# Optimization experiments

Hardware: AMD Instinct MI355X
Metric: run time of the kernel (lower is better)

Reference implementation:

```python
import jax, jax.numpy as jnp
import numpy as np

K = 3   # spatial_kernel_size
M = 5   # memory_size


def setup_inputs() -> dict:
    key = jax.random.key(0)
    ks = jax.random.split(key, 16)
    C = 64
    B, H, D, W = 2, 24, 24, 24
    s = 0.05
    n = jax.random.normal
    return {
        "x": n(ks[0], (B, C, H, D, W), jnp.float32),
        "prev_memory": jnp.zeros((B, C), jnp.float32),
        "Wq": n(ks[1], (C, C), jnp.float32) * s,
        "bq": n(ks[2], (C,), jnp.float32) * s,
        "Wk": n(ks[3], (C, C), jnp.float32) * s,
        "bk": n(ks[4], (C,), jnp.float32) * s,
        "Wv": n(ks[5], (C, C), jnp.float32) * s,
        "bv": n(ks[6], (C,), jnp.float32) * s,
        "mem_key": n(ks[7], (C, M), jnp.float32),
        "mem_value": n(ks[8], (C, M), jnp.float32),
        "Wg": n(ks[9], (C, 2 * C), jnp.float32) * s,
        "bg": n(ks[10], (C,), jnp.float32) * s,
        "W_ih": n(ks[11], (3 * C, C), jnp.float32) * s,
        "W_hh": n(ks[12], (3 * C, C), jnp.float32) * s,
        "b_ih": n(ks[13], (3 * C,), jnp.float32) * s,
        "b_hh": n(ks[14], (3 * C,), jnp.float32) * s,
    }


def _patches(x, k):
    # x: (B,C,H,D,W) -> (B,C,k^3,H,D,W) local neighborhoods (zero-padded)
    B, C, H, D, W = x.shape
    p = k // 2
    xp = jnp.pad(x, ((0, 0), (0, 0), (p, p), (p, p), (p, p)))
    sl = [xp[:, :, i:i + H, j:j + D, l:l + W]
          for i in range(k) for j in range(k) for l in range(k)]
    return jnp.stack(sl, axis=2)


def reference(x, prev_memory, Wq, bq, Wk, bk, Wv, bv, mem_key, mem_value,
              Wg, bg, W_ih, W_hh, b_ih, b_hh):
    B, C, H, D, W = x.shape
    N = H * D * W
    xf = x.reshape(B, C, N)
    pf = _patches(x, K).reshape(B, C, K ** 3, N)

    # 1x1x1 conv projections (pure channel mixes)
    q = jnp.einsum('oc,bcn->bon', Wq, xf) + bq[None, :, None]            # (B,C,N)
    k_sp = jnp.einsum('oc,bcmn->bomn', Wk, pf) + bk[None, :, None, None]  # (B,C,27,N)
    v_sp = jnp.einsum('oc,bcmn->bomn', Wv, pf) + bv[None, :, None, None]

    # memory tokens broadcast over all spatial locations
    k_mem = jnp.broadcast_to(mem_key[None, :, :, None], (B, C, M, N))
    v_mem = jnp.broadcast_to(mem_value[None, :, :, None], (B, C, M, N))
    kk = jnp.concatenate([k_mem, k_sp], axis=2)   # (B,C,M+27,N)
    vv = jnp.concatenate([v_mem, v_sp], axis=2)

    # per-channel scalar attention over memory+neighborhood axis
    attn = jax.nn.softmax(q[:, :, None, :] * kk / jnp.sqrt(jnp.float32(C)), axis=2)
    out = jnp.sum(attn * vv, axis=2).reshape(B, C, H, D, W)

    # sigmoid gate over concat([x, out])
    gin = jnp.concatenate([xf, out.reshape(B, C, N)], axis=1)  # (B,2C,N)
    gate = jax.nn.sigmoid(jnp.einsum('oc,bcn->bon', Wg, gin)
                          + bg[None, :, None]).reshape(B, C, H, D, W)
    out = gate * out + (1.0 - gate) * x

    # GRU memory update on spatially pooled features (torch GRUCell math)
    mu = out.mean(axis=(2, 3, 4))                 # (B,C)
    gi = mu @ W_ih.T + b_ih
    gh = prev_memory @ W_hh.T + b_hh
    ir, iz, ii = jnp.split(gi, 3, axis=1)
    hr, hz, hn = jnp.split(gh, 3, axis=1)
    r = jax.nn.sigmoid(ir + hr)
    z = jax.nn.sigmoid(iz + hz)
    ng = jnp.tanh(ii + r * hn)
    new_memory = (1.0 - z) * ng + z * prev_memory
    return out, new_memory
```

## Files before the change

### kernel.cpp

```cpp
#include <hip/hip_runtime.h>
#include <math.h>

#define NPOS 13824
#define CDIM 64
#define BTCH 2
#define LOG2E 1.4426950408889634f
#define QSCALE (0.125f * LOG2E)

__device__ __forceinline__ unsigned int f2bf1(float f) {
  unsigned int u = __float_as_uint(f);
  return (u + 0x7FFFu + ((u >> 16) & 1u)) >> 16;
}

__global__ __launch_bounds__(256) void qkvg_kernel(
    const float* __restrict__ x,
    const float* __restrict__ Wq, const float* __restrict__ bq,
    const float* __restrict__ Wk, const float* __restrict__ bk,
    const float* __restrict__ Wv, const float* __restrict__ bv,
    const float* __restrict__ Wg,
    unsigned int* __restrict__ KVp, float* __restrict__ QGX,
    float* __restrict__ pool)
{
  __shared__ __align__(16) float wqt[64*68];
  __shared__ __align__(16) float wkt[64*68];
  __shared__ __align__(16) float wvt[64*68];
  __shared__ __align__(16) float wgt[64*68];
  const int t  = threadIdx.x;
  const int bi = blockIdx.x;
  const int b  = bi / 216;
  const int n0 = (bi - b*216) * 64;
  if (bi == 0 && t < 128) pool[t] = 0.0f;

  #pragma unroll
  for (int k = 0; k < 16; ++k) {
    int idx = t + k*256;
    int lo = idx & 63, hi = idx >> 6;
    wqt[lo*68 + hi] = Wq[idx] * QSCALE;
    wkt[lo*68 + hi] = Wk[idx];
    wvt[lo*68 + hi] = Wv[idx];
    wgt[lo*68 + hi] = Wg[hi*128 + lo];
  }
  __syncthreads();

  const int c0  = (t & 15) * 4;
  const int nn0 = (t >> 4) * 4;
  const float* xbase = x + (size_t)(b*64)*NPOS + n0 + nn0;
  float aq[4][4] = {}; float ak[4][4] = {}; float av[4][4] = {}; float ag[4][4] = {};
  #pragma unroll 4
  for (int cp = 0; cp < 64; ++cp) {
    const float4 xv4 = *(const float4*)(xbase + (size_t)cp*NPOS);
    const float4 q4  = *(const float4*)&wqt[cp*68 + c0];
    const float4 k4  = *(const float4*)&wkt[cp*68 + c0];
    const float4 v4  = *(const float4*)&wvt[cp*68 + c0];
    const float4 g4  = *(const float4*)&wgt[cp*68 + c0];
    const float xa[4] = {xv4.x, xv4.y, xv4.z, xv4.w};
    const float qa[4] = {q4.x, q4.y, q4.z, q4.w};
    const float ka[4] = {k4.x, k4.y, k4.z, k4.w};
    const float va[4] = {v4.x, v4.y, v4.z, v4.w};
    const float ga[4] = {g4.x, g4.y, g4.z, g4.w};
    #pragma unroll
    for (int ci = 0; ci < 4; ++ci)
      #pragma unroll
      for (int ni = 0; ni < 4; ++ni) {
        aq[ci][ni] = fmaf(qa[ci], xa[ni], aq[ci][ni]);
        ak[ci][ni] = fmaf(ka[ci], xa[ni], ak[ci][ni]);
        av[ci][ni] = fmaf(va[ci], xa[ni], av[ci][ni]);
        ag[ci][ni] = fmaf(ga[ci], xa[ni], ag[ci][ni]);
      }
  }
  float4 xr[4];
  #pragma unroll
  for (int e = 0; e < 4; ++e)
    xr[e] = *(const float4*)(x + (size_t)(b*64 + c0 + e)*NPOS + n0 + nn0);
  const float xre[4][4] = {{xr[0].x,xr[0].y,xr[0].z,xr[0].w},
                           {xr[1].x,xr[1].y,xr[1].z,xr[1].w},
                           {xr[2].x,xr[2].y,xr[2].z,xr[2].w},
                           {xr[3].x,xr[3].y,xr[3].z,xr[3].w}};
  const float4 bq4 = *(const float4*)&bq[c0];
  const float4 bk4 = *(const float4*)&bk[c0];
  const float4 bv4 = *(const float4*)&bv[c0];
  const float bqa[4] = {bq4.x, bq4.y, bq4.z, bq4.w};
  const float bka[4] = {bk4.x, bk4.y, bk4.z, bk4.w};
  const float bva[4] = {bv4.x, bv4.y, bv4.z, bv4.w};
  #pragma unroll
  for (int ni = 0; ni < 4; ++ni) {
    const int p = b*NPOS + n0 + nn0 + ni;
    uint4 kv;
    kv.x = (f2bf1(ak[0][ni]+bka[0]) << 16) | f2bf1(av[0][ni]+bva[0]);
    kv.y = (f2bf1(ak[1][ni]+bka[1]) << 16) | f2bf1(av[1][ni]+bva[1]);
    kv.z = (f2bf1(ak[2][ni]+bka[2]) << 16) | f2bf1(av[2][ni]+bva[2]);
    kv.w = (f2bf1(ak[3][ni]+bka[3]) << 16) | f2bf1(av[3][ni]+bva[3]);
    *(uint4*)&KVp[p*64 + c0] = kv;
    unsigned pk0 = (f2bf1(fmaf(bqa[0], QSCALE, aq[0][ni])) << 16) | f2bf1(ag[0][ni]);
    unsigned pk1 = (f2bf1(fmaf(bqa[1], QSCALE, aq[1][ni])) << 16) | f2bf1(ag[1][ni]);
    unsigned pk2 = (f2bf1(fmaf(bqa[2], QSCALE, aq[2][ni])) << 16) | f2bf1(ag[2][ni]);
    unsigned pk3 = (f2bf1(fmaf(bqa[3], QSCALE, aq[3][ni])) << 16) | f2bf1(ag[3][ni]);
    float4 o;
    o = make_float4(__uint_as_float(pk0), xre[0][ni], __uint_as_float(pk1), xre[1][ni]);
    *(float4*)&QGX[(size_t)(p*64 + c0)*2]     = o;
    o = make_float4(__uint_as_float(pk2), xre[2][ni], __uint_as_float(pk3), xre[3][ni]);
    *(float4*)&QGX[(size_t)(p*64 + c0)*2 + 4] = o;
  }
}

__global__ __launch_bounds__(256) void attn_kernel(
    float* __restrict__ OT,
    const unsigned int* __restrict__ KVp,
    const float* __restrict__ QGX,
    const float* __restrict__ bk, const float* __restrict__ bv,
    const float* __restrict__ memk, const float* __restrict__ memv,
    const float* __restrict__ Wg, const float* __restrict__ bg,
    float* __restrict__ pool)
{
  __shared__ __align__(16) unsigned int kvbuf[64*129];
  __shared__ __align__(16) float alsA[256];
  __shared__ __align__(16) float alsB[256];
  const int t = threadIdx.x;
  const int c = t & 63;
  const int w = t >> 6;

  {
    float* wgt2 = (float*)kvbuf;
    #pragma unroll
    for (int k = 0; k < 16; ++k) {
      int u = t + k*256;
      int cp = u >> 6, j = u & 63;
      wgt2[j*65 + cp] = Wg[cp*128 + 64 + j];
    }
  }
  __syncthreads();
  unsigned int wg2p[32];
  {
    const float* wgt2 = (const float*)kvbuf;
    #pragma unroll
    for (int j2 = 0; j2 < 32; ++j2) {
      unsigned lo = f2bf1(wgt2[(2*j2)*65 + c]);
      unsigned hi = f2bf1(wgt2[(2*j2+1)*65 + c]);
      wg2p[j2] = lo | (hi << 16);
    }
  }
  float mk[5], mv[5];
  #pragma unroll
  for (int m = 0; m < 5; ++m) { mk[m] = memk[c*5 + m]; mv[m] = memv[c*5 + m]; }
  const float bg_c = bg[c];
  const unsigned bias_kv = (f2bf1(bk[c]) << 16) | f2bf1(bv[c]);
  __syncthreads();

  const int bi = (int)(blockIdx.x & 7) * 128 + (int)(blockIdx.x >> 3);
  const int b  = bi >> 9;
  const int tb = bi & 511;
  const int h0 = (tb >> 6) * 3;
  const int d0 = ((tb >> 3) & 7) * 3;
  const int w0 = (tb & 7) * 3;
  const int bN = b * NPOS;

  for (int u = t; u < 8000; u += 256) {
    const int pos = u >> 6;
    const int ph = pos / 25, pr = pos - ph*25;
    const int pd = pr / 5,  pw = pr - pd*5;
    const int hh = h0 - 1 + ph, dd = d0 - 1 + pd, ww = w0 - 1 + pw;
    const bool inb = ((unsigned)hh < 24u) && ((unsigned)dd < 24u) && ((unsigned)ww < 24u);
    unsigned kv = bias_kv;
    if (inb) kv = KVp[(size_t)(bN + hh*576 + dd*24 + ww)*64 + c];
    kvbuf[c*129 + pos] = kv;
  }
  __syncthreads();

  float pacc = 0.0f;
  for (int li = w; li < 27; li += 8) {
    const int liB0 = li + 4;
    const bool hasB = liB0 < 27;
    const int liB = hasB ? liB0 : li;

    const int lhA = li / 9,  lrA = li - lhA*9;
    const int ldA = lrA / 3, lwA = lrA - ldA*3;
    const int pA  = bN + (h0+lhA)*576 + (d0+ldA)*24 + (w0+lwA);
    const unsigned int* kvA = &kvbuf[c*129 + lhA*25 + ldA*5 + lwA];
    const int lhB = liB / 9,  lrB = liB - lhB*9;
    const int ldB = lrB / 3,  lwB = lrB - ldB*3;
    const int pB  = bN + (h0+lhB)*576 + (d0+ldB)*24 + (w0+lwB);
    const unsigned int* kvB = &kvbuf[c*129 + lhB*25 + ldB*5 + lwB];

    const float2 gqA = *(const float2*)&QGX[(size_t)(pA*64 + c)*2];
    const float2 gqB = *(const float2*)&QGX[(size_t)(pB*64 + c)*2];
    const unsigned uqA = __float_as_uint(gqA.x);
    const unsigned uqB = __float_as_uint(gqB.x);
    const float qA  = __uint_as_float(uqA & 0xFFFF0000u);
    const float gxA = __uint_as_float(uqA << 16);
    const float xvA = gqA.y;
    const float qB  = __uint_as_float(uqB & 0xFFFF0000u);
    const float gxB = __uint_as_float(uqB << 16);
    const float xvB = gqB.y;

    float sA0 = 0.f, sA1 = 0.f, oA0 = 0.f, oA1 = 0.f;
    float sB0 = 0.f, sB1 = 0.f, oB0 = 0.f, oB1 = 0.f;
    #pragma unroll
    for (int m = 0; m < 5; ++m) {
      const float pfA = __builtin_amdgcn_exp2f(qA * mk[m]);
      const float pfB = __builtin_amdgcn_exp2f(qB * mk[m]);
      if (m & 1) { sA1 += pfA; oA1 = fmaf(pfA, mv[m], oA1);
                   sB1 += pfB; oB1 = fmaf(pfB, mv[m], oB1); }
      else       { sA0 += pfA; oA0 = fmaf(pfA, mv[m], oA0);
                   sB0 += pfB; oB0 = fmaf(pfB, mv[m], oB0); }
    }
    #pragma unroll
    for (int i = 0; i < 3; ++i)
      #pragma unroll
      for (int j = 0; j < 3; ++j)
        #pragma unroll
        for (int l = 0; l < 3; ++l) {
          const int s4  = i*9 + j*3 + l;
          const int off = i*25 + j*5 + l;
          const unsigned a = kvA[off], bb2 = kvB[off];
          const float kA = __uint_as_float(a & 0xFFFF0000u);
          const float vA = __uint_as_float(a << 16);
          const float kB = __uint_as_float(bb2 & 0xFFFF0000u);
          const float vB = __uint_as_float(bb2 << 16);
          const float pfA = __builtin_amdgcn_exp2f(qA * kA);
          const float pfB = __builtin_amdgcn_exp2f(qB * kB);
          if (s4 & 1) { sA1 += pfA; oA1 = fmaf(pfA, vA, oA1);
                        sB1 += pfB; oB1 = fmaf(pfB, vB, oB1); }
          else        { sA0 += pfA; oA0 = fmaf(pfA, vA, oA0);
                        sB0 += pfB; oB0 = fmaf(pfB, vB, oB0); }
        }
    const float attA = (oA0 + oA1) * __builtin_amdgcn_rcpf(sA0 + sA1);
    const float attB = (oB0 + oB1) * __builtin_amdgcn_rcpf(sB0 + sB1);

    alsA[w*64 + c] = attA;
    alsB[w*64 + c] = attB;
    float gA0 = gxA + bg_c, gA1 = 0.f, gA2 = 0.f, gA3 = 0.f;
    float gB0 = gxB + bg_c, gB1 = 0.f, gB2 = 0.f, gB3 = 0.f;
    #pragma unroll
    for (int j4 = 0; j4 < 16; ++j4) {
      const float4 a4 = *(const float4*)&alsA[w*64 + j4*4];
      const float4 b4 = *(const float4*)&alsB[w*64 + j4*4];
      const unsigned pk0 = wg2p[2*j4], pk1 = wg2p[2*j4+1];
      const float w0f = __uint_as_float(pk0 << 16);
      const float w1f = __uint_as_float(pk0 & 0xFFFF0000u);
      const float w2f = __uint_as_float(pk1 << 16);
      const float w3f = __uint_as_float(pk1 & 0xFFFF0000u);
      gA0 = fmaf(w0f, a4.x, gA0); gB0 = fmaf(w0f, b4.x, gB0);
      gA1 = fmaf(w1f, a4.y, gA1); gB1 = fmaf(w1f, b4.y, gB1);
      gA2 = fmaf(w2f, a4.z, gA2); gB2 = fmaf(w2f, b4.z, gB2);
      gA3 = fmaf(w3f, a4.w, gA3); gB3 = fmaf(w3f, b4.w, gB3);
    }
    const float glA   = (gA0 + gA1) + (gA2 + gA3);
    const float glB   = (gB0 + gB1) + (gB2 + gB3);
    const float gateA = __builtin_amdgcn_rcpf(1.0f + __builtin_amdgcn_exp2f(-LOG2E * glA));
    const float gateB = __builtin_amdgcn_rcpf(1.0f + __builtin_amdgcn_exp2f(-LOG2E * glB));
    const float finA  = fmaf(gateA, attA - xvA, xvA);
    const float finB  = fmaf(gateB, attB - xvB, xvB);
    OT[pA*64 + c] = finA;
    pacc += finA;
    if (hasB) { OT[pB*64 + c] = finB; pacc += finB; }
  }

  alsA[t] = pacc;
  __syncthreads();
  if (t < 64) {
    float s = alsA[t] + alsA[64 + t] + alsA[128 + t] + alsA[192 + t];
    atomicAdd(&pool[b*64 + t], s);
  }
}

__global__ __launch_bounds__(256) void outpool_kernel(
    const float* __restrict__ OT, float* __restrict__ out,
    const float* __restrict__ pool, const float* __restrict__ prev,
    const float* __restrict__ W_ih, const float* __restrict__ W_hh,
    const float* __restrict__ b_ih, const float* __restrict__ b_hh,
    float* __restrict__ outmem)
{
  __shared__ __align__(16) float ls[64*65];
  __shared__ __align__(16) float mu[128];
  __shared__ float gi[384];
  __shared__ float gh[384];
  const int t  = threadIdx.x;
  const int bi = blockIdx.x;
  const int b  = bi / 216;
  const int n0 = (bi - b*216) * 64;
  #pragma unroll
  for (int i = 0; i < 16; ++i) {
    int u = i*256 + t;
    int pos = u >> 6, cc = u & 63;
    ls[cc*65 + pos] = OT[(size_t)(b*NPOS + n0 + pos)*64 + cc];
  }
  if (bi == 0 && t < 128) mu[t] = pool[t] * (1.0f / (float)NPOS);
  __syncthreads();
  #pragma unroll
  for (int i = 0; i < 16; ++i) {
    int u = i*256 + t;
    int cc = u >> 6, j = u & 63;
    out[(size_t)(b*64 + cc)*NPOS + n0 + j] = ls[cc*65 + j];
  }
  if (bi != 0) return;

  for (int r = t; r < 384; r += 256) {
    const int b2 = r / 192, j = r - b2*192;
    const float4* wi4 = (const float4*)(W_ih + (size_t)j*64);
    const float4* wh4 = (const float4*)(W_hh + (size_t)j*64);
    const float4* mu4 = (const float4*)(mu + b2*64);
    const float4* pv4 = (const float4*)(prev + b2*64);
    float sgi = b_ih[j], sgh = b_hh[j];
    #pragma unroll
    for (int k = 0; k < 16; ++k) {
      float4 wv = wi4[k], m4 = mu4[k];
      sgi = fmaf(wv.x, m4.x, sgi); sgi = fmaf(wv.y, m4.y, sgi);
      sgi = fmaf(wv.z, m4.z, sgi); sgi = fmaf(wv.w, m4.w, sgi);
      float4 hv = wh4[k], p4 = pv4[k];
      sgh = fmaf(hv.x, p4.x, sgh); sgh = fmaf(hv.y, p4.y, sgh);
      sgh = fmaf(hv.z, p4.z, sgh); sgh = fmaf(hv.w, p4.w, sgh);
    }
    gi[r] = sgi; gh[r] = sgh;
  }
  __syncthreads();
  if (t < 128) {
    const int b2 = t >> 6, cc = t & 63;
    float ir = gi[b2*192 + cc],       hr = gh[b2*192 + cc];
    float iz = gi[b2*192 + 64 + cc],  hz = gh[b2*192 + 64 + cc];
    float ii = gi[b2*192 + 128 + cc], hn = gh[b2*192 + 128 + cc];
    float rr = 1.0f / (1.0f + __builtin_amdgcn_exp2f(-LOG2E * (ir + hr)));
    float zz = 1.0f / (1.0f + __builtin_amdgcn_exp2f(-LOG2E * (iz + hz)));
    float ng = tanhf(ii + rr * hn);
    outmem[t] = (1.0f - zz) * ng + zz * prev[t];
  }
}

extern "C" void kernel_launch(void* const* d_in, const int* in_sizes, int n_in,
                              void* d_out, int out_size, void* d_ws, size_t ws_size,
                              hipStream_t stream) {
  const float* x    = (const float*)d_in[0];
  const float* prev = (const float*)d_in[1];
  const float* Wq   = (const float*)d_in[2];
  const float* bq   = (const float*)d_in[3];
  const float* Wk   = (const float*)d_in[4];
  const float* bk   = (const float*)d_in[5];
  const float* Wv   = (const float*)d_in[6];
  const float* bv   = (const float*)d_in[7];
  const float* memk = (const float*)d_in[8];
  const float* memv = (const float*)d_in[9];
  const float* Wg   = (const float*)d_in[10];
  const float* bg   = (const float*)d_in[11];
  const float* W_ih = (const float*)d_in[12];
  const float* W_hh = (const float*)d_in[13];
  const float* b_ih = (const float*)d_in[14];
  const float* b_hh = (const float*)d_in[15];

  float* out    = (float*)d_out;
  float* outmem = out + (size_t)BTCH*CDIM*NPOS;

  const size_t SZ = (size_t)BTCH*NPOS*CDIM;
  float* wsf        = (float*)d_ws;
  float* OT         = wsf;
  unsigned int* KVp = (unsigned int*)(wsf + SZ);
  float* QGX        = wsf + 2*SZ;
  float* pool       = wsf + 4*SZ;

  qkvg_kernel<<<BTCH*216, 256, 0, stream>>>(x, Wq, bq, Wk, bk, Wv, bv, Wg,
                                            KVp, QGX, pool);
  attn_kernel<<<BTCH*512, 256, 0, stream>>>(OT, KVp, QGX,
                                            bk, bv, memk, memv, Wg, bg, pool);
  outpool_kernel<<<BTCH*216, 256, 0, stream>>>(OT, out, pool, prev,
                                               W_ih, W_hh, b_ih, b_hh, outmem);
}
```

Measured before the change: 165.7 us.

## Move gate matmul from attention kernel into tiled output kernel with last-block GRU

Removes the per-position gate GEMV, weight packing and pooling from the attention kernel, which now only writes raw attention outputs. A new output kernel does the gate projection as a register-tiled 64x64 matmul from shared memory, applies the gated blend against x, writes the output in channel-major order and accumulates the pool sum. The GRU update runs in the last block to finish, detected with an atomic counter, replacing the separate block-0 path. The query and x-gate are now stored as fp32 in separate buffers instead of packed bf16, which adds memory traffic but raises precision and takes the gate work off the attention kernel.

```diff
diff --git a/kernel.cpp b/kernel.cpp
--- a/kernel.cpp
+++ b/kernel.cpp
@@ -18,8 +18,8 @@
     const float* __restrict__ Wk, const float* __restrict__ bk,
     const float* __restrict__ Wv, const float* __restrict__ bv,
     const float* __restrict__ Wg,
-    unsigned int* __restrict__ KVp, float* __restrict__ QGX,
-    float* __restrict__ pool)
+    unsigned int* __restrict__ KVp, float* __restrict__ Qs,
+    float* __restrict__ GXCN, float* __restrict__ pool)
 {
   __shared__ __align__(16) float wqt[64*68];
   __shared__ __align__(16) float wkt[64*68];
@@ -29,7 +29,7 @@
   const int bi = blockIdx.x;
   const int b  = bi / 216;
   const int n0 = (bi - b*216) * 64;
-  if (bi == 0 && t < 128) pool[t] = 0.0f;
+  if (bi == 0 && t < 132) pool[t] = 0.0f;
 
   #pragma unroll
   for (int k = 0; k < 16; ++k) {
@@ -68,14 +68,6 @@
         ag[ci][ni] = fmaf(ga[ci], xa[ni], ag[ci][ni]);
       }
   }
-  float4 xr[4];
-  #pragma unroll
-  for (int e = 0; e < 4; ++e)
-    xr[e] = *(const float4*)(x + (size_t)(b*64 + c0 + e)*NPOS + n0 + nn0);
-  const float xre[4][4] = {{xr[0].x,xr[0].y,xr[0].z,xr[0].w},
-                           {xr[1].x,xr[1].y,xr[1].z,xr[1].w},
-                           {xr[2].x,xr[2].y,xr[2].z,xr[2].w},
-                           {xr[3].x,xr[3].y,xr[3].z,xr[3].w}};
   const float4 bq4 = *(const float4*)&bq[c0];
   const float4 bk4 = *(const float4*)&bk[c0];
   const float4 bv4 = *(const float4*)&bv[c0];
@@ -85,66 +77,39 @@
   #pragma unroll
   for (int ni = 0; ni < 4; ++ni) {
     const int p = b*NPOS + n0 + nn0 + ni;
+    float4 o;
+    o = make_float4(fmaf(bqa[0],QSCALE,aq[0][ni]), fmaf(bqa[1],QSCALE,aq[1][ni]),
+                    fmaf(bqa[2],QSCALE,aq[2][ni]), fmaf(bqa[3],QSCALE,aq[3][ni]));
+    *(float4*)&Qs[p*64 + c0] = o;
     uint4 kv;
     kv.x = (f2bf1(ak[0][ni]+bka[0]) << 16) | f2bf1(av[0][ni]+bva[0]);
     kv.y = (f2bf1(ak[1][ni]+bka[1]) << 16) | f2bf1(av[1][ni]+bva[1]);
     kv.z = (f2bf1(ak[2][ni]+bka[2]) << 16) | f2bf1(av[2][ni]+bva[2]);
     kv.w = (f2bf1(ak[3][ni]+bka[3]) << 16) | f2bf1(av[3][ni]+bva[3]);
     *(uint4*)&KVp[p*64 + c0] = kv;
-    unsigned pk0 = (f2bf1(fmaf(bqa[0], QSCALE, aq[0][ni])) << 16) | f2bf1(ag[0][ni]);
-    unsigned pk1 = (f2bf1(fmaf(bqa[1], QSCALE, aq[1][ni])) << 16) | f2bf1(ag[1][ni]);
-    unsigned pk2 = (f2bf1(fmaf(bqa[2], QSCALE, aq[2][ni])) << 16) | f2bf1(ag[2][ni]);
-    unsigned pk3 = (f2bf1(fmaf(bqa[3], QSCALE, aq[3][ni])) << 16) | f2bf1(ag[3][ni]);
-    float4 o;
-    o = make_float4(__uint_as_float(pk0), xre[0][ni], __uint_as_float(pk1), xre[1][ni]);
-    *(float4*)&QGX[(size_t)(p*64 + c0)*2]     = o;
-    o = make_float4(__uint_as_float(pk2), xre[2][ni], __uint_as_float(pk3), xre[3][ni]);
-    *(float4*)&QGX[(size_t)(p*64 + c0)*2 + 4] = o;
-  }
+  }
+  #pragma unroll
+  for (int ci = 0; ci < 4; ++ci)
+    *(float4*)&GXCN[(size_t)(b*64 + c0 + ci)*NPOS + n0 + nn0] =
+        make_float4(ag[ci][0], ag[ci][1], ag[ci][2], ag[ci][3]);
 }
 
 __global__ __launch_bounds__(256) void attn_kernel(
-    float* __restrict__ OT,
+    float* __restrict__ ATT,
+    const float* __restrict__ Qs,
     const unsigned int* __restrict__ KVp,
-    const float* __restrict__ QGX,
     const float* __restrict__ bk, const float* __restrict__ bv,
-    const float* __restrict__ memk, const float* __restrict__ memv,
-    const float* __restrict__ Wg, const float* __restrict__ bg,
-    float* __restrict__ pool)
+    const float* __restrict__ memk, const float* __restrict__ memv)
 {
   __shared__ __align__(16) unsigned int kvbuf[64*129];
-  __shared__ __align__(16) float alsA[256];
-  __shared__ __align__(16) float alsB[256];
   const int t = threadIdx.x;
   const int c = t & 63;
   const int w = t >> 6;
 
-  {
-    float* wgt2 = (float*)kvbuf;
-    #pragma unroll
-    for (int k = 0; k < 16; ++k) {
-      int u = t + k*256;
-      int cp = u >> 6, j = u & 63;
-      wgt2[j*65 + cp] = Wg[cp*128 + 64 + j];
-    }
-  }
-  __syncthreads();
-  unsigned int wg2p[32];
-  {
-    const float* wgt2 = (const float*)kvbuf;
-    #pragma unroll
-    for (int j2 = 0; j2 < 32; ++j2) {
-      unsigned lo = f2bf1(wgt2[(2*j2)*65 + c]);
-      unsigned hi = f2bf1(wgt2[(2*j2+1)*65 + c]);
-      wg2p[j2] = lo | (hi << 16);
-    }
-  }
   float mk[5], mv[5];
   #pragma unroll
   for (int m = 0; m < 5; ++m) { mk[m] = memk[c*5 + m]; mv[m] = memv[c*5 + m]; }
-  const float bg_c = bg[c];
   const unsigned bias_kv = (f2bf1(bk[c]) << 16) | f2bf1(bv[c]);
-  __syncthreads();
 
   const int bi = (int)(blockIdx.x & 7) * 128 + (int)(blockIdx.x >> 3);
   const int b  = bi >> 9;
@@ -166,7 +131,6 @@
   }
   __syncthreads();
 
-  float pacc = 0.0f;
   for (int li = w; li < 27; li += 8) {
     const int liB0 = li + 4;
     const bool hasB = liB0 < 27;
@@ -181,16 +145,8 @@
     const int pB  = bN + (h0+lhB)*576 + (d0+ldB)*24 + (w0+lwB);
     const unsigned int* kvB = &kvbuf[c*129 + lhB*25 + ldB*5 + lwB];
 
-    const float2 gqA = *(const float2*)&QGX[(size_t)(pA*64 + c)*2];
-    const float2 gqB = *(const float2*)&QGX[(size_t)(pB*64 + c)*2];
-    const unsigned uqA = __float_as_uint(gqA.x);
-    const unsigned uqB = __float_as_uint(gqB.x);
-    const float qA  = __uint_as_float(uqA & 0xFFFF0000u);
-    const float gxA = __uint_as_float(uqA << 16);
-    const float xvA = gqA.y;
-    const float qB  = __uint_as_float(uqB & 0xFFFF0000u);
-    const float gxB = __uint_as_float(uqB << 16);
-    const float xvB = gqB.y;
+    const float qA = Qs[pA*64 + c];
+    const float qB = Qs[pB*64 + c];
 
     float sA0 = 0.f, sA1 = 0.f, oA0 = 0.f, oA1 = 0.f;
     float sB0 = 0.f, sB1 = 0.f, oB0 = 0.f, oB1 = 0.f;
@@ -225,103 +181,133 @@
         }
     const float attA = (oA0 + oA1) * __builtin_amdgcn_rcpf(sA0 + sA1);
     const float attB = (oB0 + oB1) * __builtin_amdgcn_rcpf(sB0 + sB1);
-
-    alsA[w*64 + c] = attA;
-    alsB[w*64 + c] = attB;
-    float gA0 = gxA + bg_c, gA1 = 0.f, gA2 = 0.f, gA3 = 0.f;
-    float gB0 = gxB + bg_c, gB1 = 0.f, gB2 = 0.f, gB3 = 0.f;
-    #pragma unroll
-    for (int j4 = 0; j4 < 16; ++j4) {
-      const float4 a4 = *(const float4*)&alsA[w*64 + j4*4];
-      const float4 b4 = *(const float4*)&alsB[w*64 + j4*4];
-      const unsigned pk0 = wg2p[2*j4], pk1 = wg2p[2*j4+1];
-      const float w0f = __uint_as_float(pk0 << 16);
-      const float w1f = __uint_as_float(pk0 & 0xFFFF0000u);
-      const float w2f = __uint_as_float(pk1 << 16);
-      const float w3f = __uint_as_float(pk1 & 0xFFFF0000u);
-      gA0 = fmaf(w0f, a4.x, gA0); gB0 = fmaf(w0f, b4.x, gB0);
-      gA1 = fmaf(w1f, a4.y, gA1); gB1 = fmaf(w1f, b4.y, gB1);
-      gA2 = fmaf(w2f, a4.z, gA2); gB2 = fmaf(w2f, b4.z, gB2);
-      gA3 = fmaf(w3f, a4.w, gA3); gB3 = fmaf(w3f, b4.w, gB3);
-    }
-    const float glA   = (gA0 + gA1) + (gA2 + gA3);
-    const float glB   = (gB0 + gB1) + (gB2 + gB3);
-    const float gateA = __builtin_amdgcn_rcpf(1.0f + __builtin_amdgcn_exp2f(-LOG2E * glA));
-    const float gateB = __builtin_amdgcn_rcpf(1.0f + __builtin_amdgcn_exp2f(-LOG2E * glB));
-    const float finA  = fmaf(gateA, attA - xvA, xvA);
-    const float finB  = fmaf(gateB, attB - xvB, xvB);
-    OT[pA*64 + c] = finA;
-    pacc += finA;
-    if (hasB) { OT[pB*64 + c] = finB; pacc += finB; }
-  }
-
-  alsA[t] = pacc;
-  __syncthreads();
-  if (t < 64) {
-    float s = alsA[t] + alsA[64 + t] + alsA[128 + t] + alsA[192 + t];
-    atomicAdd(&pool[b*64 + t], s);
-  }
-}
-
-__global__ __launch_bounds__(256) void outpool_kernel(
-    const float* __restrict__ OT, float* __restrict__ out,
-    const float* __restrict__ pool, const float* __restrict__ prev,
+    ATT[pA*64 + c] = attA;
+    if (hasB) ATT[pB*64 + c] = attB;
+  }
+}
+
+__global__ __launch_bounds__(256) void gateout_kernel(
+    const float* __restrict__ ATT, const float* __restrict__ GXCN,
+    const float* __restrict__ x, const float* __restrict__ Wg,
+    const float* __restrict__ bg,
+    float* __restrict__ out, float* __restrict__ pool, int* __restrict__ cnt,
+    const float* __restrict__ prev,
     const float* __restrict__ W_ih, const float* __restrict__ W_hh,
     const float* __restrict__ b_ih, const float* __restrict__ b_hh,
     float* __restrict__ outmem)
 {
-  __shared__ __align__(16) float ls[64*65];
+  __shared__ __align__(16) float wgt[64*68];
+  __shared__ __align__(16) float ats[64*68];
+  __shared__ __align__(16) float psum[1024];
   __shared__ __align__(16) float mu[128];
   __shared__ float gi[384];
   __shared__ float gh[384];
+  __shared__ int flag;
   const int t  = threadIdx.x;
   const int bi = blockIdx.x;
   const int b  = bi / 216;
   const int n0 = (bi - b*216) * 64;
-  #pragma unroll
-  for (int i = 0; i < 16; ++i) {
-    int u = i*256 + t;
+  const int bN = b * NPOS;
+  if (t == 0) flag = 0;
+
+  #pragma unroll
+  for (int k = 0; k < 16; ++k) {
+    int u = t + k*256;
+    int cp = u & 63, co = u >> 6;
+    wgt[cp*68 + co] = Wg[co*128 + 64 + cp];
     int pos = u >> 6, cc = u & 63;
-    ls[cc*65 + pos] = OT[(size_t)(b*NPOS + n0 + pos)*64 + cc];
-  }
-  if (bi == 0 && t < 128) mu[t] = pool[t] * (1.0f / (float)NPOS);
-  __syncthreads();
-  #pragma unroll
-  for (int i = 0; i < 16; ++i) {
-    int u = i*256 + t;
-    int cc = u >> 6, j = u & 63;
-    out[(size_t)(b*64 + cc)*NPOS + n0 + j] = ls[cc*65 + j];
-  }
-  if (bi != 0) return;
-
-  for (int r = t; r < 384; r += 256) {
-    const int b2 = r / 192, j = r - b2*192;
-    const float4* wi4 = (const float4*)(W_ih + (size_t)j*64);
-    const float4* wh4 = (const float4*)(W_hh + (size_t)j*64);
-    const float4* mu4 = (const float4*)(mu + b2*64);
-    const float4* pv4 = (const float4*)(prev + b2*64);
-    float sgi = b_ih[j], sgh = b_hh[j];
-    #pragma unroll
-    for (int k = 0; k < 16; ++k) {
-      float4 wv = wi4[k], m4 = mu4[k];
-      sgi = fmaf(wv.x, m4.x, sgi); sgi = fmaf(wv.y, m4.y, sgi);
-      sgi = fmaf(wv.z, m4.z, sgi); sgi = fmaf(wv.w, m4.w, sgi);
-      float4 hv = wh4[k], p4 = pv4[k];
-      sgh = fmaf(hv.x, p4.x, sgh); sgh = fmaf(hv.y, p4.y, sgh);
-      sgh = fmaf(hv.z, p4.z, sgh); sgh = fmaf(hv.w, p4.w, sgh);
+    ats[cc*68 + pos] = ATT[(size_t)(bN + n0 + pos)*64 + cc];
+  }
+  __syncthreads();
+
+  const int c0  = (t & 15) * 4;
+  const int nn0 = (t >> 4) * 4;
+  const float4 bg4 = *(const float4*)&bg[c0];
+  float g[4][4];
+  #pragma unroll
+  for (int ci = 0; ci < 4; ++ci) {
+    const float4 gx4 = *(const float4*)&GXCN[(size_t)(b*64 + c0 + ci)*NPOS + n0 + nn0];
+    const float bgc = (ci == 0) ? bg4.x : (ci == 1) ? bg4.y : (ci == 2) ? bg4.z : bg4.w;
+    g[ci][0] = gx4.x + bgc; g[ci][1] = gx4.y + bgc;
+    g[ci][2] = gx4.z + bgc; g[ci][3] = gx4.w + bgc;
+  }
+  #pragma unroll 4
+  for (int cp = 0; cp < 64; ++cp) {
+    const float4 w4 = *(const float4*)&wgt[cp*68 + c0];
+    const float4 a4 = *(const float4*)&ats[cp*68 + nn0];
+    const float wa[4] = {w4.x, w4.y, w4.z, w4.w};
+    const float aa[4] = {a4.x, a4.y, a4.z, a4.w};
+    #pragma unroll
+    for (int ci = 0; ci < 4; ++ci)
+      #pragma unroll
+      for (int ni = 0; ni < 4; ++ni)
+        g[ci][ni] = fmaf(wa[ci], aa[ni], g[ci][ni]);
+  }
+  #pragma unroll
+  for (int ci = 0; ci < 4; ++ci) {
+    const size_t row = (size_t)(b*64 + c0 + ci)*NPOS + n0 + nn0;
+    const float4 x4 = *(const float4*)(x + row);
+    const float4 a4 = *(const float4*)&ats[(c0 + ci)*68 + nn0];
+    const float xa[4] = {x4.x, x4.y, x4.z, x4.w};
+    const float aa[4] = {a4.x, a4.y, a4.z, a4.w};
+    float fin[4], s = 0.0f;
+    #pragma unroll
+    for (int ni = 0; ni < 4; ++ni) {
+      const float gate = __builtin_amdgcn_rcpf(
+          1.0f + __builtin_amdgcn_exp2f(-LOG2E * g[ci][ni]));
+      fin[ni] = fmaf(gate, aa[ni] - xa[ni], xa[ni]);
+      s += fin[ni];
     }
-    gi[r] = sgi; gh[r] = sgh;
-  }
-  __syncthreads();
-  if (t < 128) {
-    const int b2 = t >> 6, cc = t & 63;
-    float ir = gi[b2*192 + cc],       hr = gh[b2*192 + cc];
-    float iz = gi[b2*192 + 64 + cc],  hz = gh[b2*192 + 64 + cc];
-    float ii = gi[b2*192 + 128 + cc], hn = gh[b2*192 + 128 + cc];
-    float rr = 1.0f / (1.0f + __builtin_amdgcn_exp2f(-LOG2E * (ir + hr)));
-    float zz = 1.0f / (1.0f + __builtin_amdgcn_exp2f(-LOG2E * (iz + hz)));
-    float ng = tanhf(ii + rr * hn);
-    outmem[t] = (1.0f - zz) * ng + zz * prev[t];
+    *(float4*)(out + row) = make_float4(fin[0], fin[1], fin[2], fin[3]);
+    psum[t*4 + ci] = s;
+  }
+  __syncthreads();
+  if (t < 64) {
+    float s = 0.0f;
+    #pragma unroll
+    for (int k = 0; k < 16; ++k) s += psum[k*64 + t];
+    atomicAdd(&pool[b*64 + t], s);
+  }
+  if (t == 0) {
+    __threadfence();
+    if (atomicAdd(cnt, 1) == (int)gridDim.x - 1) flag = 1;
+  }
+  __syncthreads();
+
+  if (flag) {
+    if (t < 128)
+      mu[t] = __hip_atomic_load(&pool[t], __ATOMIC_RELAXED,
+                                __HIP_MEMORY_SCOPE_AGENT) * (1.0f / (float)NPOS);
+    __syncthreads();
+    for (int r = t; r < 384; r += 256) {
+      const int b2 = r / 192, j = r - b2*192;
+      const float4* wi4 = (const float4*)(W_ih + (size_t)j*64);
+      const float4* wh4 = (const float4*)(W_hh + (size_t)j*64);
+      const float4* mu4 = (const float4*)(mu + b2*64);
+      const float4* pv4 = (const float4*)(prev + b2*64);
+      float sgi = b_ih[j], sgh = b_hh[j];
+      #pragma unroll
+      for (int k = 0; k < 16; ++k) {
+        float4 wv = wi4[k], m4 = mu4[k];
+        sgi = fmaf(wv.x, m4.x, sgi); sgi = fmaf(wv.y, m4.y, sgi);
+        sgi = fmaf(wv.z, m4.z, sgi); sgi = fmaf(wv.w, m4.w, sgi);
+        float4 hv = wh4[k], p4 = pv4[k];
+        sgh = fmaf(hv.x, p4.x, sgh); sgh = fmaf(hv.y, p4.y, sgh);
+        sgh = fmaf(hv.z, p4.z, sgh); sgh = fmaf(hv.w, p4.w, sgh);
+      }
+      gi[r] = sgi; gh[r] = sgh;
+    }
+    __syncthreads();
+    if (t < 128) {
+      const int b2 = t >> 6, cc = t & 63;
+      float ir = gi[b2*192 + cc],       hr = gh[b2*192 + cc];
+      float iz = gi[b2*192 + 64 + cc],  hz = gh[b2*192 + 64 + cc];
+      float ii = gi[b2*192 + 128 + cc], hn = gh[b2*192 + 128 + cc];
+      float rr = 1.0f / (1.0f + __builtin_amdgcn_exp2f(-LOG2E * (ir + hr)));
+      float zz = 1.0f / (1.0f + __builtin_amdgcn_exp2f(-LOG2E * (iz + hz)));
+      float ng = tanhf(ii + rr * hn);
+      outmem[t] = (1.0f - zz) * ng + zz * prev[t];
+    }
   }
 }
 
@@ -350,15 +336,17 @@
 
   const size_t SZ = (size_t)BTCH*NPOS*CDIM;
   float* wsf        = (float*)d_ws;
-  float* OT         = wsf;
+  float* ATT        = wsf;
   unsigned int* KVp = (unsigned int*)(wsf + SZ);
-  float* QGX        = wsf + 2*SZ;
+  float* Qs         = wsf + 2*SZ;
+  float* GXCN       = wsf + 3*SZ;
   float* pool       = wsf + 4*SZ;
+  int*   cnt        = (int*)(pool + 128);
 
   qkvg_kernel<<<BTCH*216, 256, 0, stream>>>(x, Wq, bq, Wk, bk, Wv, bv, Wg,
-                                            KVp, QGX, pool);
-  attn_kernel<<<BTCH*512, 256, 0, stream>>>(OT, KVp, QGX,
-                                            bk, bv, memk, memv, Wg, bg, pool);
-  outpool_kernel<<<BTCH*216, 256, 0, stream>>>(OT, out, pool, prev,
+                                            KVp, Qs, GXCN, pool);
+  attn_kernel<<<BTCH*512, 256, 0, stream>>>(ATT, Qs, KVp, bk, bv, memk, memv);
+  gateout_kernel<<<BTCH*216, 256, 0, stream>>>(ATT, GXCN, x, Wg, bg,
+                                               out, pool, cnt, prev,
                                                W_ih, W_hh, b_ih, b_hh, outmem);
 }
```

Measured after the change: 161.2 us. -2.7%, faster.
